# Optimization experiments

Hardware: AMD Instinct MI355X
Metric: run time of the kernel (lower is better)

The kernel has to match this reference:

```python
import jax, jax.numpy as jnp
import numpy as np

B, S, D = 2, 2048, 2560
H, HKV, HD = 8, 4, 256
EPS = 1e-6
SCALING = 256 ** -0.5          # query_pre_attn_scalar ** -0.5
SOFTCAP = 4096.0               # sliding_window passed positionally into softcap slot
NEG = -1e9


def rms_norm(x, w):
    # x: [..., HD]; computed in fp32 like the torch module
    xf = x.astype(jnp.float32)
    out = xf * jax.lax.rsqrt(jnp.mean(xf * xf, axis=-1, keepdims=True) + EPS)
    return (out * (1.0 + w.astype(jnp.float32))).astype(x.dtype)


def rotate_half(x):
    x1, x2 = x[..., : HD // 2], x[..., HD // 2:]
    return jnp.concatenate((-x2, x1), axis=-1)


def apply_rope(x, cos, sin):
    # cos/sin: [B, S, HD] -> broadcast over head axis 1
    c, s = cos[:, None], sin[:, None]
    return x * c + rotate_half(x) * s


def setup_inputs() -> dict:
    key = jax.random.key(0)
    ks = jax.random.split(key, 6)
    x = jax.random.normal(ks[0], (B, S, D), dtype=jnp.float32)
    # RoPE angles (theta=10000, linear scaling factor 8)
    inv_freq = 1.0 / (10000.0 ** (np.arange(0, HD, 2, dtype=np.float32) / HD))
    pos = np.arange(S, dtype=np.float32) / 8.0
    ang = np.einsum('s,d->sd', pos, inv_freq)
    ang = np.concatenate([ang, ang], axis=-1)               # [S, HD]
    cos = jnp.asarray(np.broadcast_to(np.cos(ang), (B, S, HD)).copy())
    sin = jnp.asarray(np.broadcast_to(np.sin(ang), (B, S, HD)).copy())
    # causal additive mask [B, 1, S, S]
    causal = np.where(np.tril(np.ones((S, S), dtype=bool)), 0.0, NEG).astype(np.float32)
    mask = jnp.asarray(np.broadcast_to(causal, (B, 1, S, S)).copy())
    sc = 0.02
    q_w = jax.random.normal(ks[1], (H * HD, D), dtype=jnp.float32) * sc
    k_w = jax.random.normal(ks[2], (HKV * HD, D), dtype=jnp.float32) * sc
    v_w = jax.random.normal(ks[3], (HKV * HD, D), dtype=jnp.float32) * sc
    o_w = jax.random.normal(ks[4], (D, H * HD), dtype=jnp.float32) * sc
    qn_w = jnp.zeros((HD,), dtype=jnp.float32)
    kn_w = jnp.zeros((HD,), dtype=jnp.float32)
    return {"x": x, "cos": cos, "sin": sin, "mask": mask,
            "q_w": q_w, "k_w": k_w, "v_w": v_w, "o_w": o_w,
            "qn_w": qn_w, "kn_w": kn_w}


def reference(x, cos, sin, mask, q_w, k_w, v_w, o_w, qn_w, kn_w):
    b, s, _ = x.shape
    # projections -> [B, H(kv), S, HD]
    q = (x @ q_w.T).reshape(b, s, H, HD).transpose(0, 2, 1, 3)
    k = (x @ k_w.T).reshape(b, s, HKV, HD).transpose(0, 2, 1, 3)
    v = (x @ v_w.T).reshape(b, s, HKV, HD).transpose(0, 2, 1, 3)
    q = rms_norm(q, qn_w)
    k = rms_norm(k, kn_w)
    q = apply_rope(q, cos, sin)
    k = apply_rope(k, cos, sin)
    # GQA: repeat kv heads (interleave matches repeat_interleave on dim=1)
    rep = H // HKV
    k = jnp.repeat(k, rep, axis=1)
    v = jnp.repeat(v, rep, axis=1)
    w = jnp.einsum('bhqd,bhkd->bhqk', q, k) * SCALING
    w = jnp.tanh(w / SOFTCAP) * SOFTCAP                     # softcap (bug-faithful)
    w = w + mask[:, :, :, : k.shape[2]]
    p = jax.nn.softmax(w.astype(jnp.float32), axis=-1).astype(q.dtype)
    attn = jnp.einsum('bhqk,bhkd->bhqd', p, v)
    attn = attn.transpose(0, 2, 1, 3).reshape(b, s, H * HD)
    return attn @ o_w.T
```

## Files before the change

kernel.cpp:

```cpp
#include <hip/hip_runtime.h>
#include <hip/hip_bf16.h>

#define BB   2
#define SS   2048
#define DD   2560
#define HH   8
#define HKVV 4
#define HDD  256
#define MM   (BB*SS)
#define NQ   (HH*HDD)
#define NKV  (HKVV*HDD)
#define SCALING 0.0625f
#define SOFTCAP 4096.0f
#define CAPC    (1.0f/(3.0f*SOFTCAP*SOFTCAP))
#define M0      20.0f

typedef __attribute__((ext_vector_type(8))) short short8;
typedef __attribute__((ext_vector_type(8))) unsigned short ushort8;
typedef __attribute__((ext_vector_type(4))) unsigned short us4;
typedef __attribute__((ext_vector_type(4))) float f32x4;

__device__ __forceinline__ float bf2f(unsigned short u) {
    union { unsigned int i; float f; } v; v.i = ((unsigned int)u) << 16; return v.f;
}
__device__ __forceinline__ unsigned short f2bf(float f) {
    union { float f; unsigned int i; } v; v.f = f;
    return (unsigned short)((v.i + 0x7fffu + ((v.i >> 16) & 1u)) >> 16);
}
__device__ __forceinline__ f32x4 mfma16(short8 a, short8 b, f32x4 c) {
    return __builtin_amdgcn_mfma_f32_16x16x32_bf16(a, b, c, 0, 0, 0);
}

__device__ __forceinline__ void async_cp16(const void* g, void* l) {
    __builtin_amdgcn_global_load_lds(
        (__attribute__((address_space(1))) void*)(g),
        (__attribute__((address_space(3))) void*)(l), 16, 0, 0);
}

__device__ __forceinline__ ushort8 ld8(const unsigned short* p) { return *(const ushort8*)p; }
__device__ __forceinline__ ushort8 ld8(const float* p) {
    ushort8 r;
#pragma unroll
    for (int i = 0; i < 8; i++) r[i] = f2bf(p[i]);
    return r;
}
__device__ __forceinline__ void stc(float* p, float v)          { *p = v; }
__device__ __forceinline__ void stc(unsigned short* p, float v) { *p = f2bf(v); }
__device__ __forceinline__ void stage8(const unsigned short* src, unsigned short* lds) {
    async_cp16(src, lds);
}
__device__ __forceinline__ void stage8(const float* src, unsigned short* lds) {
    *(ushort8*)lds = ld8(src);
}

__global__ __launch_bounds__(256) void cvt_bf16(const float* __restrict__ in,
                                                unsigned short* __restrict__ out, int n4)
{
    int i = blockIdx.x * 256 + threadIdx.x;
    const int stride = gridDim.x * 256;
    for (; i < n4; i += stride) {
        float4 v = ((const float4*)in)[i];
        us4 o;
        o[0] = f2bf(v.x); o[1] = f2bf(v.y); o[2] = f2bf(v.z); o[3] = f2bf(v.w);
        ((us4*)out)[i] = o;
    }
}

__global__ __launch_bounds__(256) void cvt_w4(const float* __restrict__ s0,
                                              const float* __restrict__ s1,
                                              const float* __restrict__ s2,
                                              const float* __restrict__ s3,
                                              unsigned short* __restrict__ dst)
{
    const int y = blockIdx.y;
    const int n4q = (int)((size_t)NQ  * DD / 4);
    const int n4k = (int)((size_t)NKV * DD / 4);
    const float* src; int n4; size_t off4;
    if (y == 0)      { src = s0; n4 = n4q; off4 = 0; }
    else if (y == 1) { src = s1; n4 = n4k; off4 = (size_t)n4q; }
    else if (y == 2) { src = s2; n4 = n4k; off4 = (size_t)n4q + n4k; }
    else             { src = s3; n4 = n4q; off4 = (size_t)n4q + 2 * (size_t)n4k; }
    us4* out = (us4*)dst + off4;
    int i = blockIdx.x * 256 + threadIdx.x;
    const int stride = gridDim.x * 256;
    for (; i < n4; i += stride) {
        float4 v = ((const float4*)src)[i];
        us4 o;
        o[0] = f2bf(v.x); o[1] = f2bf(v.y); o[2] = f2bf(v.z); o[3] = f2bf(v.w);
        out[i] = o;
    }
}

template<typename TA, typename TB, typename TC, bool VT_OUT>
__global__ __launch_bounds__(256) void gemm_k(const TA* __restrict__ A,
                                              const TB* __restrict__ Bm,
                                              TC* __restrict__ C,
                                              int M, int N, int K)
{
    __shared__ __align__(16) unsigned short As[128][32];
    __shared__ __align__(16) unsigned short Bs[128][32];

    const int tid  = threadIdx.x;
    const int bm   = blockIdx.x, bn = blockIdx.y;
    const int wave = tid >> 6, lane = tid & 63;
    const int quad = lane >> 4, lm = lane & 15;
    const int wm = (wave >> 1) * 64, wn = (wave & 1) * 64;

    f32x4 acc[4][4];
#pragma unroll
    for (int i = 0; i < 4; i++)
#pragma unroll
        for (int j = 0; j < 4; j++) acc[i][j] = (f32x4)0.0f;

    unsigned short* AsF = &As[0][0];
    unsigned short* BsF = &Bs[0][0];
    const int grow = tid >> 2;
    const int gcol = (tid & 3) * 8;
    const TA* Ab = A  + (size_t)(bm * 128) * K;
    const TB* Bb = Bm + (size_t)(bn * 128) * K;

    for (int k0 = 0; k0 < K; k0 += 32) {
        stage8(&Ab[(size_t)(grow     ) * K + k0 + gcol], AsF + tid * 8);
        stage8(&Ab[(size_t)(grow + 64) * K + k0 + gcol], AsF + 2048 + tid * 8);
        stage8(&Bb[(size_t)(grow     ) * K + k0 + gcol], BsF + tid * 8);
        stage8(&Bb[(size_t)(grow + 64) * K + k0 + gcol], BsF + 2048 + tid * 8);
        __syncthreads();

        short8 af[4], bf[4];
#pragma unroll
        for (int t = 0; t < 4; t++) af[t] = *(const short8*)&As[wm + t * 16 + lm][quad * 8];
#pragma unroll
        for (int t = 0; t < 4; t++) bf[t] = *(const short8*)&Bs[wn + t * 16 + lm][quad * 8];
#pragma unroll
        for (int i = 0; i < 4; i++)
#pragma unroll
            for (int j = 0; j < 4; j++)
                acc[i][j] = mfma16(af[i], bf[j], acc[i][j]);
        __syncthreads();
    }

#pragma unroll
    for (int i = 0; i < 4; i++)
#pragma unroll
        for (int j = 0; j < 4; j++) {
            if constexpr (VT_OUT) {
                int row0 = bm * 128 + wm + i * 16 + quad * 4;
                int col  = bn * 128 + wn + j * 16 + lm;
                int b    = row0 >> 11, s0 = row0 & (SS - 1);
                int kvh  = col >> 8,   d  = col & (HDD - 1);
                us4 pk;
#pragma unroll
                for (int r = 0; r < 4; r++) pk[r] = f2bf(acc[i][j][r]);
                *(us4*)&C[(((size_t)b * HKVV + kvh) * HDD + d) * SS + s0] = pk;
            } else {
#pragma unroll
                for (int r = 0; r < 4; r++) {
                    int row = bm * 128 + wm + i * 16 + quad * 4 + r;
                    int col = bn * 128 + wn + j * 16 + lm;
                    stc(&C[(size_t)row * N + col], acc[i][j][r]);
                }
            }
        }
}

template<typename TA>
__global__ __launch_bounds__(256) void gemm_qkv(const TA* __restrict__ A,
                                                const unsigned short* __restrict__ Bm,
                                                unsigned short* __restrict__ Qo,
                                                unsigned short* __restrict__ Ko,
                                                unsigned short* __restrict__ Vo,
                                                int K)
{
    __shared__ __align__(16) unsigned short As[128][32];
    __shared__ __align__(16) unsigned short Bs[128][32];

    const int tid  = threadIdx.x;
    const int bm   = blockIdx.x, bn = blockIdx.y;
    const int wave = tid >> 6, lane = tid & 63;
    const int quad = lane >> 4, lm = lane & 15;
    const int wm = (wave >> 1) * 64, wn = (wave & 1) * 64;

    f32x4 acc[4][4];
#pragma unroll
    for (int i = 0; i < 4; i++)
#pragma unroll
        for (int j = 0; j < 4; j++) acc[i][j] = (f32x4)0.0f;

    unsigned short* AsF = &As[0][0];
    unsigned short* BsF = &Bs[0][0];
    const int grow = tid >> 2;
    const int gcol = (tid & 3) * 8;
    const TA* Ab = A  + (size_t)(bm * 128) * K;
    const unsigned short* Bb = Bm + (size_t)(bn * 128) * K;

    for (int k0 = 0; k0 < K; k0 += 32) {
        stage8(&Ab[(size_t)(grow     ) * K + k0 + gcol], AsF + tid * 8);
        stage8(&Ab[(size_t)(grow + 64) * K + k0 + gcol], AsF + 2048 + tid * 8);
        stage8(&Bb[(size_t)(grow     ) * K + k0 + gcol], BsF + tid * 8);
        stage8(&Bb[(size_t)(grow + 64) * K + k0 + gcol], BsF + 2048 + tid * 8);
        __syncthreads();

        short8 af[4], bf[4];
#pragma unroll
        for (int t = 0; t < 4; t++) af[t] = *(const short8*)&As[wm + t * 16 + lm][quad * 8];
#pragma unroll
        for (int t = 0; t < 4; t++) bf[t] = *(const short8*)&Bs[wn + t * 16 + lm][quad * 8];
#pragma unroll
        for (int i = 0; i < 4; i++)
#pragma unroll
            for (int j = 0; j < 4; j++)
                acc[i][j] = mfma16(af[i], bf[j], acc[i][j]);
        __syncthreads();
    }

#pragma unroll
    for (int i = 0; i < 4; i++)
#pragma unroll
        for (int j = 0; j < 4; j++) {
            const int row0 = bm * 128 + wm + i * 16 + quad * 4;
            const int col  = bn * 128 + wn + j * 16 + lm;
            if (col < 2048) {
#pragma unroll
                for (int r = 0; r < 4; r++)
                    Qo[(size_t)(row0 + r) * NQ + col] = f2bf(acc[i][j][r]);
            } else if (col < 3072) {
                const int ck = col - 2048;
#pragma unroll
                for (int r = 0; r < 4; r++)
                    Ko[(size_t)(row0 + r) * NKV + ck] = f2bf(acc[i][j][r]);
            } else {
                const int cv = col - 3072;
                const int b = row0 >> 11, s0 = row0 & (SS - 1);
                const int kvh = cv >> 8, d = cv & (HDD - 1);
                us4 pk;
#pragma unroll
                for (int r = 0; r < 4; r++) pk[r] = f2bf(acc[i][j][r]);
                *(us4*)&Vo[(((size_t)b * HKVV + kvh) * HDD + d) * SS + s0] = pk;
            }
        }
}

__global__ __launch_bounds__(256) void norm_rope2(unsigned short* __restrict__ Qx,
                                                  unsigned short* __restrict__ Kx,
                                                  const float* __restrict__ qnw,
                                                  const float* __restrict__ knw,
                                                  const float* __restrict__ cosb,
                                                  const float* __restrict__ sinb)
{
    const int bs = blockIdx.x;
    const int y  = blockIdx.y;
    const int t  = threadIdx.x;
    unsigned short* X; const float* nw; int nheads, h;
    if (y < HH) { X = Qx; nw = qnw; nheads = HH;   h = y; }
    else        { X = Kx; nw = knw; nheads = HKVV; h = y - HH; }

    __shared__ float xs[256];
    __shared__ float red[4];

    const size_t base = ((size_t)bs * nheads + h) * HDD;
    float v = bf2f(X[base + t]);
    xs[t] = v;

    float p = v * v;
#pragma unroll
    for (int off = 32; off >= 1; off >>= 1) p += __shfl_xor(p, off);
    if ((t & 63) == 0) red[t >> 6] = p;
    __syncthreads();
    float sum = red[0] + red[1] + red[2] + red[3];
    float rs  = rsqrtf(sum * (1.0f / HDD) + 1e-6f);

    const int pt = (t + 128) & 255;
    float w1 = 1.0f + nw[t];
    float w2 = 1.0f + nw[pt];
    float normed  = v * rs * w1;
    float partner = xs[pt] * rs * w2;
    float rot = (t < 128) ? -partner : partner;
    float c = cosb[(size_t)bs * HDD + t];
    float s = sinb[(size_t)bs * HDD + t];
    X[base + t] = f2bf(normed * c + rot * s);
}

__global__ __launch_bounds__(256) void norm_rope(unsigned short* __restrict__ X,
                                                 const float* __restrict__ nw,
                                                 const float* __restrict__ cosb,
                                                 const float* __restrict__ sinb,
                                                 int nheads)
{
    const int bs = blockIdx.x;
    const int h  = blockIdx.y;
    const int t  = threadIdx.x;

    __shared__ float xs[256];
    __shared__ float red[4];

    const size_t base = ((size_t)bs * nheads + h) * HDD;
    float v = bf2f(X[base + t]);
    xs[t] = v;

    float p = v * v;
#pragma unroll
    for (int off = 32; off >= 1; off >>= 1) p += __shfl_xor(p, off);
    if ((t & 63) == 0) red[t >> 6] = p;
    __syncthreads();
    float sum = red[0] + red[1] + red[2] + red[3];
    float rs  = rsqrtf(sum * (1.0f / HDD) + 1e-6f);

    const int pt = (t + 128) & 255;
    float w1 = 1.0f + nw[t];
    float w2 = 1.0f + nw[pt];
    float normed  = v * rs * w1;
    float partner = xs[pt] * rs * w2;
    float rot = (t < 128) ? -partner : partner;
    float c = cosb[(size_t)bs * HDD + t];
    float s = sinb[(size_t)bs * HDD + t];
    X[base + t] = f2bf(normed * c + rot * s);
}

__device__ const unsigned char unit_tbl[48] = {
    62, 124, 125, 120, 121,
    58, 116, 117, 112, 113,
    54, 108, 109, 104, 105,
    50, 100, 101,  96,  97,
    46,  92,  93,  88,  89,
    42,  84,  85,  80,  81,
    38,  76,  77,  72,  73,
    34,  68,  69,  64,  65,
    30,  26,  22,  18,  14, 10, 6, 2
};

__global__ __launch_bounds__(256) void attn_split(const unsigned short* __restrict__ Q,
                                                  const unsigned short* __restrict__ K,
                                                  const unsigned short* __restrict__ VT,
                                                  unsigned short* __restrict__ O,
                                                  float* __restrict__ Opart,
                                                  float* __restrict__ lpart)
{
    const int tid = threadIdx.x, w = tid >> 6, lane = tid & 63;
    const int quad = lane >> 4, lm = lane & 15;
    const int hb = blockIdx.x;
    const int h = hb & 7, b = hb >> 3, kvh = h >> 1;

    const unsigned int u = unit_tbl[blockIdx.y];
    const int qb = u >> 2;
    const bool single = (u & 2) != 0;
    const int half = u & 1;
    const int q0 = qb * 64;
    const int T  = 2 * (qb + 1);
    const int t_lo = (!single && half) ? (qb + 1) : 0;
    const int t_hi = single ? T : (half ? T : (qb + 1));

    __shared__ __align__(16) unsigned short Ks[2][32 * 256];
    __shared__ __align__(16) unsigned short Vt[256 * 32];
    __shared__ __align__(16) unsigned short Ps[4 * 512];

    const unsigned short* Qb = Q + (((size_t)b * SS + q0 + w * 16 + lm) * HH + h) * HDD;
    short8 qf[8];
#pragma unroll
    for (int c = 0; c < 8; c++) qf[c] = *(const short8*)&Qb[c * 32 + quad * 8];

    const unsigned short* Kb = K  + (size_t)b * SS * NKV + (size_t)kvh * HDD;
    const unsigned short* Vb = VT + ((size_t)b * HKVV + kvh) * HDD * (size_t)SS;

    f32x4 o_acc[16];
#pragma unroll
    for (int i = 0; i < 16; i++) o_acc[i] = (f32x4)0.0f;
    float l_r[4] = {0.f, 0.f, 0.f, 0.f};

    const int mylo = q0 + w * 16;
    const int row  = mylo + quad * 4;

    auto STAGE_K = [&](int bi, int k0) {
#pragma unroll
        for (int p = 0; p < 4; p++) {
            const int slot = p * 256 + tid;
            const int krow = slot >> 5, kc = slot & 31;
            async_cp16(&Kb[(size_t)(k0 + krow) * NKV + ((kc ^ (krow & 7)) * 8)],
                       &Ks[bi][slot * 8]);
        }
    };
    auto STAGE_V = [&](int k0) {
#pragma unroll
        for (int p = 0; p < 4; p++) {
            const int slot = p * 256 + tid;
            const int vd = slot >> 2, vc = slot & 3;
            async_cp16(&Vb[(size_t)vd * SS + k0 + ((vc ^ ((vd >> 1) & 3)) * 8)],
                       &Vt[slot * 8]);
        }
    };

    STAGE_K(0, t_lo * 32);
    STAGE_V(t_lo * 32);
    int cur = 0;

    for (int t = t_lo; t < t_hi; t++) {
        const int k0 = t * 32;
        const bool more = (t + 1 < t_hi);

        if (more) {
            STAGE_K(cur ^ 1, k0 + 32);
            asm volatile("s_waitcnt vmcnt(8)" ::: "memory");
        } else {
            asm volatile("s_waitcnt vmcnt(4)" ::: "memory");
        }
        __builtin_amdgcn_s_barrier();
        __builtin_amdgcn_sched_barrier(0);

        short8 pf;
        if (k0 <= mylo + 15) {
            f32x4 sa0 = (f32x4)0.0f, sa1 = (f32x4)0.0f;
            __builtin_amdgcn_s_setprio(1);
#pragma unroll
            for (int c = 0; c < 8; c++) {
                const int cs = (((c * 4 + quad) ^ (lm & 7))) * 8;
                short8 kf0 = *(const short8*)&Ks[cur][lm * 256 + cs];
                short8 kf1 = *(const short8*)&Ks[cur][(16 + lm) * 256 + cs];
                sa0 = mfma16(qf[c], kf0, sa0);
                sa1 = mfma16(qf[c], kf1, sa1);
            }
            __builtin_amdgcn_s_setprio(0);

            const bool msk = (k0 + 31 > mylo);
            float pe[2][4];
#pragma unroll
            for (int t2 = 0; t2 < 2; t2++) {
                const int key = k0 + t2 * 16 + lm;
#pragma unroll
                for (int r = 0; r < 4; r++) {
                    float s = (t2 ? sa1[r] : sa0[r]) * SCALING;
                    s = s - s * s * s * CAPC;
                    float e = __expf(s - M0);
                    if (msk && key > row + r) e = 0.0f;
                    pe[t2][r] = e;
                    l_r[r] += e;
                }
            }

#pragma unroll
            for (int t2 = 0; t2 < 2; t2++)
#pragma unroll
                for (int r = 0; r < 4; r++) {
                    const int g = (t2 * 2 + (lm >> 3)) ^ r ^ quad;
                    Ps[w * 512 + (quad * 4 + r) * 32 + g * 8 + (lm & 7)] = f2bf(pe[t2][r]);
                }
            asm volatile("s_waitcnt lgkmcnt(0)" ::: "memory");
            __builtin_amdgcn_sched_barrier(0);
            const int gr = quad ^ (lm & 3) ^ (lm >> 2);
            pf = *(const short8*)&Ps[w * 512 + lm * 32 + gr * 8];
        }

        if (more) asm volatile("s_waitcnt vmcnt(4)" ::: "memory");
        else      asm volatile("s_waitcnt vmcnt(0)" ::: "memory");
        __builtin_amdgcn_s_barrier();
        __builtin_amdgcn_sched_barrier(0);

        if (k0 <= mylo + 15) {
            __builtin_amdgcn_s_setprio(1);
#pragma unroll
            for (int nt = 0; nt < 16; nt++) {
                short8 vf = *(const short8*)&Vt[(nt * 16 + lm) * 32
                                                + ((quad ^ ((lm >> 1) & 3)) * 8)];
                o_acc[nt] = mfma16(pf, vf, o_acc[nt]);
            }
            __builtin_amdgcn_s_setprio(0);
        }

        __builtin_amdgcn_sched_barrier(0);
        __builtin_amdgcn_s_barrier();
        __builtin_amdgcn_sched_barrier(0);
        if (more) STAGE_V(k0 + 32);
        cur ^= 1;
    }

#pragma unroll
    for (int off = 1; off < 16; off <<= 1)
#pragma unroll
        for (int r = 0; r < 4; r++) l_r[r] += __shfl_xor(l_r[r], off);

    if (single) {
#pragma unroll
        for (int r = 0; r < 4; r++) {
            float inv = 1.0f / l_r[r];
            unsigned short* Ob = O + ((size_t)b * SS + row + r) * NQ + h * HDD;
#pragma unroll
            for (int nt = 0; nt < 16; nt++)
                Ob[nt * 16 + lm] = f2bf(o_acc[nt][r] * inv);
        }
    } else {
        const int slot = (((b * HH + h) * 16 + (qb - 16)) << 1) | half;
        float* Ob = Opart + ((size_t)slot * 64 + w * 16 + quad * 4) * 256;
#pragma unroll
        for (int r = 0; r < 4; r++) {
            if (lm == 0) lpart[slot * 64 + w * 16 + quad * 4 + r] = l_r[r];
#pragma unroll
            for (int nt = 0; nt < 16; nt++)
                Ob[(size_t)r * 256 + nt * 16 + lm] = o_acc[nt][r];
        }
    }
}

__global__ __launch_bounds__(256) void attn_reduce(const float* __restrict__ Op,
                                                   const float* __restrict__ lp,
                                                   unsigned short* __restrict__ ATT)
{
    const int sp  = blockIdx.x >> 4;
    const int wr0 = (blockIdx.x & 15) * 4;
    const int r   = threadIdx.x >> 6;
    const int c0  = (threadIdx.x & 63) * 4;
    const int wrow = wr0 + r;
    const int qbm = sp & 15, h = (sp >> 4) & 7, b = sp >> 7;

    const size_t base0 = ((size_t)(sp * 2) * 64 + wrow) * 256;
    const size_t base1 = base0 + (size_t)64 * 256;
    float4 a = *(const float4*)&Op[base0 + c0];
    float4 d = *(const float4*)&Op[base1 + c0];
    float l = lp[sp * 2 * 64 + wrow] + lp[(sp * 2 + 1) * 64 + wrow];
    float inv = 1.0f / l;
    us4 o;
    o[0] = f2bf((a.x + d.x) * inv); o[1] = f2bf((a.y + d.y) * inv);
    o[2] = f2bf((a.z + d.z) * inv); o[3] = f2bf((a.w + d.w) * inv);
    const int srow = (16 + qbm) * 64 + wrow;
    *(us4*)&ATT[(((size_t)b * SS + srow) * HH + h) * HDD + c0] = o;
}

__global__ __launch_bounds__(256) void attn_kernel(const unsigned short* __restrict__ Q,
                                                   const unsigned short* __restrict__ K,
                                                   const unsigned short* __restrict__ VT,
                                                   unsigned short* __restrict__ O)
{
    const int tid = threadIdx.x, w = tid >> 6, lane = tid & 63;
    const int quad = lane >> 4, lm = lane & 15;
    const int h = blockIdx.y, b = blockIdx.z, kvh = h >> 1;

    const int bx = blockIdx.x;
    const int qb = (bx & 1) ? (31 - (bx >> 1)) : (bx >> 1);
    const int q0 = qb * 64;
    const int T  = 2 * (qb + 1);

    __shared__ __align__(16) unsigned short Ks[2][32 * 256];
    __shared__ __align__(16) unsigned short Vt[2][256 * 32];
    __shared__ __align__(16) unsigned short Ps[4 * 512];

    const unsigned short* Qb = Q + (((size_t)b * SS + q0 + w * 16 + lm) * HH + h) * HDD;
    short8 qf[8];
#pragma unroll
    for (int c = 0; c < 8; c++) qf[c] = *(const short8*)&Qb[c * 32 + quad * 8];

    const unsigned short* Kb = K  + (size_t)b * SS * NKV + (size_t)kvh * HDD;
    const unsigned short* Vb = VT + ((size_t)b * HKVV + kvh) * HDD * (size_t)SS;

    f32x4 o_acc[16];
#pragma unroll
    for (int i = 0; i < 16; i++) o_acc[i] = (f32x4)0.0f;
    float l_r[4] = {0.f, 0.f, 0.f, 0.f};

    const int mylo = q0 + w * 16;
    const int row  = mylo + quad * 4;

    auto STAGE = [&](int bi, int k0) {
#pragma unroll
        for (int p = 0; p < 4; p++) {
            const int slot = p * 256 + tid;
            const int krow = slot >> 5, kc = slot & 31;
            async_cp16(&Kb[(size_t)(k0 + krow) * NKV + ((kc ^ (krow & 7)) * 8)],
                       &Ks[bi][slot * 8]);
            const int vd = slot >> 2, vc = slot & 3;
            async_cp16(&Vb[(size_t)vd * SS + k0 + ((vc ^ ((vd >> 1) & 3)) * 8)],
                       &Vt[bi][slot * 8]);
        }
    };

    STAGE(0, 0);
    int cur = 0;

    for (int t = 0; t < T; t++) {
        const int k0 = t * 32;

        if (t + 1 < T) {
            STAGE(cur ^ 1, k0 + 32);
            asm volatile("s_waitcnt vmcnt(8)" ::: "memory");
        } else {
            asm volatile("s_waitcnt vmcnt(0)" ::: "memory");
        }
        __builtin_amdgcn_s_barrier();
        __builtin_amdgcn_sched_barrier(0);

        if (k0 <= mylo + 15) {
            f32x4 sa0 = (f32x4)0.0f, sa1 = (f32x4)0.0f;
            __builtin_amdgcn_s_setprio(1);
#pragma unroll
            for (int c = 0; c < 8; c++) {
                const int cs = (((c * 4 + quad) ^ (lm & 7))) * 8;
                short8 kf0 = *(const short8*)&Ks[cur][lm * 256 + cs];
                short8 kf1 = *(const short8*)&Ks[cur][(16 + lm) * 256 + cs];
                sa0 = mfma16(qf[c], kf0, sa0);
                sa1 = mfma16(qf[c], kf1, sa1);
            }
            __builtin_amdgcn_s_setprio(0);

            const bool msk = (k0 + 31 > mylo);
            float pe[2][4];
#pragma unroll
            for (int t2 = 0; t2 < 2; t2++) {
                const int key = k0 + t2 * 16 + lm;
#pragma unroll
                for (int r = 0; r < 4; r++) {
                    float s = (t2 ? sa1[r] : sa0[r]) * SCALING;
                    s = s - s * s * s * CAPC;
                    float e = __expf(s - M0);
                    if (msk && key > row + r) e = 0.0f;
                    pe[t2][r] = e;
                    l_r[r] += e;
                }
            }

#pragma unroll
            for (int t2 = 0; t2 < 2; t2++)
#pragma unroll
                for (int r = 0; r < 4; r++) {
                    const int g = (t2 * 2 + (lm >> 3)) ^ r ^ quad;
                    Ps[w * 512 + (quad * 4 + r) * 32 + g * 8 + (lm & 7)] = f2bf(pe[t2][r]);
                }
            asm volatile("s_waitcnt lgkmcnt(0)" ::: "memory");
            __builtin_amdgcn_sched_barrier(0);
            const int gr = quad ^ (lm & 3) ^ (lm >> 2);
            short8 pf = *(const short8*)&Ps[w * 512 + lm * 32 + gr * 8];

            __builtin_amdgcn_s_setprio(1);
#pragma unroll
            for (int nt = 0; nt < 16; nt++) {
                short8 vf = *(const short8*)&Vt[cur][(nt * 16 + lm) * 32
                                                    + ((quad ^ ((lm >> 1) & 3)) * 8)];
                o_acc[nt] = mfma16(pf, vf, o_acc[nt]);
            }
            __builtin_amdgcn_s_setprio(0);
        }

        __builtin_amdgcn_sched_barrier(0);
        __builtin_amdgcn_s_barrier();
        __builtin_amdgcn_sched_barrier(0);
        cur ^= 1;
    }

#pragma unroll
    for (int off = 1; off < 16; off <<= 1)
#pragma unroll
        for (int r = 0; r < 4; r++) l_r[r] += __shfl_xor(l_r[r], off);
#pragma unroll
    for (int r = 0; r < 4; r++) {
        float inv = 1.0f / l_r[r];
        unsigned short* Ob = O + ((size_t)b * SS + row + r) * NQ + h * HDD;
#pragma unroll
        for (int nt = 0; nt < 16; nt++)
            Ob[nt * 16 + lm] = f2bf(o_acc[nt][r] * inv);
    }
}

extern "C" void kernel_launch(void* const* d_in, const int* in_sizes, int n_in,
                              void* d_out, int out_size, void* d_ws, size_t ws_size,
                              hipStream_t stream)
{
    const float* x    = (const float*)d_in[0];
    const float* cosb = (const float*)d_in[1];
    const float* sinb = (const float*)d_in[2];
    const float* q_w  = (const float*)d_in[4];
    const float* k_w  = (const float*)d_in[5];
    const float* v_w  = (const float*)d_in[6];
    const float* o_w  = (const float*)d_in[7];
    const float* qn_w = (const float*)d_in[8];
    const float* kn_w = (const float*)d_in[9];
    float* out = (float*)d_out;

    const size_t sz_xb = (size_t)MM * DD;
    const size_t sz_wq = (size_t)NQ * DD;
    const size_t sz_wk = (size_t)NKV * DD;
    const size_t sz_q  = (size_t)MM * NQ;
    const size_t sz_k  = (size_t)MM * NKV;

    const size_t needA = (sz_xb + 2 * sz_wq + 2 * sz_wk + sz_q + 2 * sz_k) * 2;
    const size_t needB = (2 * sz_wq + 2 * sz_wk + sz_q + 2 * sz_k) * 2;

    if (ws_size >= needA) {
        unsigned short* xb  = (unsigned short*)d_ws;
        unsigned short* wqb = xb  + sz_xb;
        unsigned short* wkb = wqb + sz_wq;
        unsigned short* wvb = wkb + sz_wk;
        unsigned short* wob = wvb + sz_wk;
        unsigned short* Qw  = wob + sz_wq;
        unsigned short* Kw  = Qw  + sz_q;
        unsigned short* VTw = Kw  + sz_k;
        float* Opart = (float*)d_ws;
        float* lpart = Opart + (size_t)512 * 64 * 256;
        unsigned short* ATT = Qw;

        cvt_bf16<<<2048, 256, 0, stream>>>(x, xb, (int)(sz_xb / 4));
        cvt_w4<<<dim3(512, 4), 256, 0, stream>>>(q_w, k_w, v_w, o_w, wqb);

        gemm_qkv<unsigned short>
            <<<dim3(MM/128, 4096/128), 256, 0, stream>>>(xb, wqb, Qw, Kw, VTw, DD);

        norm_rope2<<<dim3(MM, HH + HKVV), 256, 0, stream>>>(Qw, Kw, qn_w, kn_w, cosb, sinb);

        attn_split<<<dim3(16, 48), 256, 0, stream>>>(Qw, Kw, VTw, ATT, Opart, lpart);
        attn_reduce<<<4096, 256, 0, stream>>>(Opart, lpart, ATT);

        gemm_k<unsigned short, unsigned short, float, false>
            <<<dim3(MM/128, DD/128), 256, 0, stream>>>(ATT, wob, out, MM, DD, NQ);
    } else if (ws_size >= needB) {
        unsigned short* wqb = (unsigned short*)d_ws;
        unsigned short* wkb = wqb + sz_wq;
        unsigned short* wvb = wkb + sz_wk;
        unsigned short* wob = wvb + sz_wk;
        unsigned short* Qw  = wob + sz_wq;
        unsigned short* Kw  = Qw  + sz_q;
        unsigned short* VTw = Kw  + sz_k;
        unsigned short* ATT = wqb;

        cvt_w4<<<dim3(512, 4), 256, 0, stream>>>(q_w, k_w, v_w, o_w, wqb);

        gemm_qkv<float>
            <<<dim3(MM/128, 4096/128), 256, 0, stream>>>(x, wqb, Qw, Kw, VTw, DD);

        norm_rope2<<<dim3(MM, HH + HKVV), 256, 0, stream>>>(Qw, Kw, qn_w, kn_w, cosb, sinb);

        attn_kernel<<<dim3(32, HH, BB), 256, 0, stream>>>(Qw, Kw, VTw, ATT);

        gemm_k<unsigned short, unsigned short, float, false>
            <<<dim3(MM/128, DD/128), 256, 0, stream>>>(ATT, wob, out, MM, DD, NQ);
    } else {
        unsigned short* Qw  = (unsigned short*)d_ws;
        unsigned short* Kw  = Qw  + sz_q;
        unsigned short* VTw = Kw  + sz_k;
        unsigned short* ATT = VTw + sz_k;

        gemm_k<float, float, unsigned short, false>
            <<<dim3(MM/128, NQ /128), 256, 0, stream>>>(x, q_w, Qw,  MM, NQ,  DD);
        gemm_k<float, float, unsigned short, false>
            <<<dim3(MM/128, NKV/128), 256, 0, stream>>>(x, k_w, Kw,  MM, NKV, DD);
        gemm_k<float, float, unsigned short, true>
            <<<dim3(MM/128, NKV/128), 256, 0, stream>>>(x, v_w, VTw, MM, NKV, DD);

        norm_rope<<<dim3(MM, HH),   256, 0, stream>>>(Qw, qn_w, cosb, sinb, HH);
        norm_rope<<<dim3(MM, HKVV), 256, 0, stream>>>(Kw, kn_w, cosb, sinb, HKVV);

        attn_kernel<<<dim3(32, HH, BB), 256, 0, stream>>>(Qw, Kw, VTw, ATT);

        gemm_k<unsigned short, float, float, false>
            <<<dim3(MM/128, DD/128), 256, 0, stream>>>(ATT, o_w, out, MM, DD, NQ);
    }
}
```

Measured before the change: 487.4 us.

## Replace QKV projection GEMM with 256x256 double-buffered async-copy kernel

Adds a new QKV projection kernel using 256x256 output tiles, 512 threads, BK=64, swizzled LDS layout and double-buffered asynchronous global-to-LDS copies with explicit waitcnt and priority hints. It replaces the 128x128 single-buffered kernel to raise data reuse per tile and overlap loads with MFMA work. The trade-offs are 128KB of LDS per block, higher register pressure and fewer blocks (256 total), which may reduce occupancy and SM fill on a large GPU.

```diff
diff --git a/kernel.cpp b/kernel.cpp
--- a/kernel.cpp
+++ b/kernel.cpp
@@ -163,6 +163,145 @@
         }
 }
 
+__global__ __launch_bounds__(512, 2) void gemm_qkv256(const unsigned short* __restrict__ A,
+                                                      const unsigned short* __restrict__ Bm,
+                                                      unsigned short* __restrict__ Qo,
+                                                      unsigned short* __restrict__ Ko,
+                                                      unsigned short* __restrict__ Vo,
+                                                      int K)
+{
+    __shared__ __align__(16) unsigned short Asm[2][256 * 64];
+    __shared__ __align__(16) unsigned short Bsm[2][256 * 64];
+
+    const int tid  = threadIdx.x;
+    const int wid  = tid >> 6, lane = tid & 63;
+    const int quad = lane >> 4, lm = lane & 15;
+    const int wr   = wid >> 2, wc = wid & 3;
+    const int bm   = blockIdx.x, bn = blockIdx.y;
+
+    f32x4 acc[8][4];
+#pragma unroll
+    for (int i = 0; i < 8; i++)
+#pragma unroll
+        for (int j = 0; j < 4; j++) acc[i][j] = (f32x4)0.0f;
+
+    const unsigned short* Ab = A  + (size_t)(bm * 256) * K;
+    const unsigned short* Bb = Bm + (size_t)(bn * 256) * K;
+
+    auto STAGE = [&](int buf, int k0) {
+#pragma unroll
+        for (int p = 0; p < 4; p++) {
+            const int slot = p * 512 + tid;
+            const int row = slot >> 3, ch = slot & 7;
+            async_cp16(&Ab[(size_t)row * K + k0 + ((ch ^ (row & 7)) * 8)],
+                       &Asm[buf][slot * 8]);
+        }
+#pragma unroll
+        for (int p = 0; p < 4; p++) {
+            const int slot = p * 512 + tid;
+            const int row = slot >> 3, ch = slot & 7;
+            async_cp16(&Bb[(size_t)row * K + k0 + ((ch ^ (row & 7)) * 8)],
+                       &Bsm[buf][slot * 8]);
+        }
+    };
+
+#define QKV_PHASE(MH, NH)                                                         \
+    do {                                                                          \
+        short8 a_[4][2], b_[2][2];                                                \
+        _Pragma("unroll")                                                         \
+        for (int mi = 0; mi < 4; mi++) {                                          \
+            const int arow = wr * 128 + ((MH) * 4 + mi) * 16 + lm;                \
+            _Pragma("unroll")                                                     \
+            for (int ks = 0; ks < 2; ks++)                                        \
+                a_[mi][ks] = *(const short8*)&Asm[cur][arow * 64 +                \
+                                (((ks * 4 + quad) ^ (arow & 7)) * 8)];            \
+        }                                                                         \
+        _Pragma("unroll")                                                         \
+        for (int ni = 0; ni < 2; ni++) {                                          \
+            const int brow = wc * 64 + ((NH) * 2 + ni) * 16 + lm;                 \
+            _Pragma("unroll")                                                     \
+            for (int ks = 0; ks < 2; ks++)                                        \
+                b_[ni][ks] = *(const short8*)&Bsm[cur][brow * 64 +                \
+                                (((ks * 4 + quad) ^ (brow & 7)) * 8)];            \
+        }                                                                         \
+        asm volatile("s_waitcnt lgkmcnt(0)" ::: "memory");                        \
+        __builtin_amdgcn_sched_barrier(0);                                        \
+        __builtin_amdgcn_s_setprio(1);                                            \
+        _Pragma("unroll")                                                         \
+        for (int mi = 0; mi < 4; mi++)                                            \
+            _Pragma("unroll")                                                     \
+            for (int ni = 0; ni < 2; ni++)                                        \
+                _Pragma("unroll")                                                 \
+                for (int ks = 0; ks < 2; ks++)                                    \
+                    acc[(MH) * 4 + mi][(NH) * 2 + ni] =                           \
+                        mfma16(a_[mi][ks], b_[ni][ks],                            \
+                               acc[(MH) * 4 + mi][(NH) * 2 + ni]);                \
+        __builtin_amdgcn_s_setprio(0);                                            \
+        __builtin_amdgcn_s_barrier();                                             \
+        __builtin_amdgcn_sched_barrier(0);                                        \
+    } while (0)
+
+    const int NT = K >> 6;
+    STAGE(0, 0);
+    int cur = 0;
+
+    for (int t = 0; t < NT; t++) {
+        if (t + 1 < NT) {
+            STAGE(cur ^ 1, (t + 1) * 64);
+            asm volatile("s_waitcnt vmcnt(8)" ::: "memory");
+        } else {
+            asm volatile("s_waitcnt vmcnt(0)" ::: "memory");
+        }
+        __builtin_amdgcn_s_barrier();
+        __builtin_amdgcn_sched_barrier(0);
+
+        QKV_PHASE(0, 0);
+        QKV_PHASE(0, 1);
+        QKV_PHASE(1, 0);
+        QKV_PHASE(1, 1);
+        cur ^= 1;
+    }
+#undef QKV_PHASE
+
+    if (bn < 8) {
+#pragma unroll
+        for (int m = 0; m < 8; m++)
+#pragma unroll
+            for (int n = 0; n < 4; n++) {
+                const int row0 = bm * 256 + wr * 128 + m * 16 + quad * 4;
+                const int colg = bn * 256 + wc * 64 + n * 16 + lm;
+#pragma unroll
+                for (int r = 0; r < 4; r++)
+                    Qo[(size_t)(row0 + r) * NQ + colg] = f2bf(acc[m][n][r]);
+            }
+    } else if (bn < 12) {
+#pragma unroll
+        for (int m = 0; m < 8; m++)
+#pragma unroll
+            for (int n = 0; n < 4; n++) {
+                const int row0 = bm * 256 + wr * 128 + m * 16 + quad * 4;
+                const int ck   = bn * 256 + wc * 64 + n * 16 + lm - 2048;
+#pragma unroll
+                for (int r = 0; r < 4; r++)
+                    Ko[(size_t)(row0 + r) * NKV + ck] = f2bf(acc[m][n][r]);
+            }
+    } else {
+#pragma unroll
+        for (int m = 0; m < 8; m++)
+#pragma unroll
+            for (int n = 0; n < 4; n++) {
+                const int row0 = bm * 256 + wr * 128 + m * 16 + quad * 4;
+                const int cv   = bn * 256 + wc * 64 + n * 16 + lm - 3072;
+                const int b = row0 >> 11, s0 = row0 & (SS - 1);
+                const int kvh = cv >> 8, d = cv & (HDD - 1);
+                us4 pk;
+#pragma unroll
+                for (int r = 0; r < 4; r++) pk[r] = f2bf(acc[m][n][r]);
+                *(us4*)&Vo[(((size_t)b * HKVV + kvh) * HDD + d) * SS + s0] = pk;
+            }
+    }
+}
+
 template<typename TA>
 __global__ __launch_bounds__(256) void gemm_qkv(const TA* __restrict__ A,
                                                 const unsigned short* __restrict__ Bm,
@@ -695,8 +834,7 @@
         cvt_bf16<<<2048, 256, 0, stream>>>(x, xb, (int)(sz_xb / 4));
         cvt_w4<<<dim3(512, 4), 256, 0, stream>>>(q_w, k_w, v_w, o_w, wqb);
 
-        gemm_qkv<unsigned short>
-            <<<dim3(MM/128, 4096/128), 256, 0, stream>>>(xb, wqb, Qw, Kw, VTw, DD);
+        gemm_qkv256<<<dim3(MM/256, 4096/256), 512, 0, stream>>>(xb, wqb, Qw, Kw, VTw, DD);
 
         norm_rope2<<<dim3(MM, HH + HKVV), 256, 0, stream>>>(Qw, Kw, qn_w, kn_w, cosb, sinb);
 
```

New measurement: 457.1 us. 1.07x faster.
